# Optimization experiments

Hardware: AMD Instinct MI355X
Metric: run time of the kernel (lower is better)

## Reference

```python
import jax, jax.numpy as jnp
import numpy as np

N = 50000
E = 600000
IN_DIM = 2000
HID = 64
OUT_DIM = 25
HEADS = 4
NHEAD = 4
NLAYERS = 2
FF = 2048
EPS = 1e-5


def gat_conv(x, W, a_src, a_dst, b, src, dst, heads, out_dim):
    n = x.shape[0]
    h = (x @ W).reshape(n, heads, out_dim)
    # per-node attention logits
    al_src = jnp.sum(h * a_src[None], axis=-1)  # [N,H]
    al_dst = jnp.sum(h * a_dst[None], axis=-1)  # [N,H]
    e = jax.nn.leaky_relu(al_src[src] + al_dst[dst], negative_slope=0.2)  # [E,H]
    # segment softmax over destination nodes (every node has a self-loop)
    m = jax.ops.segment_max(e, dst, num_segments=n)
    ex = jnp.exp(e - m[dst])
    s = jax.ops.segment_sum(ex, dst, num_segments=n)
    alpha = ex / (s[dst] + 1e-16)  # [E,H]
    msg = h[src] * alpha[..., None]  # [E,H,out]
    out = jax.ops.segment_sum(msg, dst, num_segments=n)  # [N,H,out]
    return out.reshape(n, heads * out_dim) + b


def layer_norm(x, g, b):
    mu = jnp.mean(x, axis=-1, keepdims=True)
    var = jnp.mean(jnp.square(x - mu), axis=-1, keepdims=True)
    return (x - mu) * jax.lax.rsqrt(var + EPS) * g + b


def encoder_layer(x, Wq, Wk, Wv, bq, bk, bv, Wo, bo, g1, b1, Wf1, bf1, Wf2, bf2, g2, b2):
    # seq_len = 1: each node is its own length-1 sequence -> softmax weights are 1
    n, d = x.shape
    dh = d // NHEAD
    q = (x @ Wq + bq).reshape(n, NHEAD, dh)
    k = (x @ Wk + bk).reshape(n, NHEAD, dh)
    v = (x @ Wv + bv).reshape(n, NHEAD, dh)
    s = jnp.sum(q * k, axis=-1, keepdims=True) / jnp.sqrt(jnp.float32(dh))  # [N,H,1]
    a = jax.nn.softmax(s, axis=-1)  # all ones (length-1 softmax)
    attn = (a * v).reshape(n, d) @ Wo + bo
    x = layer_norm(x + attn, g1, b1)
    ff = jax.nn.relu(x @ Wf1 + bf1) @ Wf2 + bf2
    return layer_norm(x + ff, g2, b2)


def setup_inputs() -> dict:
    key = jax.random.key(0)
    ks = jax.random.split(key, 40)
    sc = 0.05
    inp = {}
    inp["x"] = jax.random.normal(ks[0], (N, IN_DIM), dtype=jnp.float32)
    inp["edge_src"] = jax.random.randint(ks[1], (E,), 0, N, dtype=jnp.int32)
    inp["edge_dst"] = jax.random.randint(ks[2], (E,), 0, N, dtype=jnp.int32)
    # GAT layer 1: in -> hidden, heads=4
    inp["W1"] = jax.random.normal(ks[3], (IN_DIM, HEADS * HID), dtype=jnp.float32) * sc
    inp["a_src1"] = jax.random.normal(ks[4], (HEADS, HID), dtype=jnp.float32) * sc
    inp["a_dst1"] = jax.random.normal(ks[5], (HEADS, HID), dtype=jnp.float32) * sc
    inp["b1"] = jnp.zeros((HEADS * HID,), dtype=jnp.float32)
    # GAT layer 2: hidden*heads -> hidden, heads=1
    inp["W2"] = jax.random.normal(ks[6], (HEADS * HID, HID), dtype=jnp.float32) * sc
    inp["a_src2"] = jax.random.normal(ks[7], (1, HID), dtype=jnp.float32) * sc
    inp["a_dst2"] = jax.random.normal(ks[8], (1, HID), dtype=jnp.float32) * sc
    inp["b2"] = jnp.zeros((HID,), dtype=jnp.float32)
    # Transformer fusion params, stacked over layers
    def pl(k, shape):
        return jax.random.normal(k, shape, dtype=jnp.float32) * sc
    inp["t_Wq"] = pl(ks[9], (NLAYERS, HID, HID))
    inp["t_Wk"] = pl(ks[10], (NLAYERS, HID, HID))
    inp["t_Wv"] = pl(ks[11], (NLAYERS, HID, HID))
    inp["t_bq"] = jnp.zeros((NLAYERS, HID), dtype=jnp.float32)
    inp["t_bk"] = jnp.zeros((NLAYERS, HID), dtype=jnp.float32)
    inp["t_bv"] = jnp.zeros((NLAYERS, HID), dtype=jnp.float32)
    inp["t_Wo"] = pl(ks[12], (NLAYERS, HID, HID))
    inp["t_bo"] = jnp.zeros((NLAYERS, HID), dtype=jnp.float32)
    inp["t_ln1g"] = jnp.ones((NLAYERS, HID), dtype=jnp.float32)
    inp["t_ln1b"] = jnp.zeros((NLAYERS, HID), dtype=jnp.float32)
    inp["t_Wff1"] = pl(ks[13], (NLAYERS, HID, FF))
    inp["t_bff1"] = jnp.zeros((NLAYERS, FF), dtype=jnp.float32)
    inp["t_Wff2"] = pl(ks[14], (NLAYERS, FF, HID))
    inp["t_bff2"] = jnp.zeros((NLAYERS, HID), dtype=jnp.float32)
    inp["t_ln2g"] = jnp.ones((NLAYERS, HID), dtype=jnp.float32)
    inp["t_ln2b"] = jnp.zeros((NLAYERS, HID), dtype=jnp.float32)
    # GAT ADT head: hidden -> out, heads=1
    inp["W3"] = pl(ks[15], (HID, OUT_DIM))
    inp["a_src3"] = pl(ks[16], (1, OUT_DIM))
    inp["a_dst3"] = pl(ks[17], (1, OUT_DIM))
    inp["b3"] = jnp.zeros((OUT_DIM,), dtype=jnp.float32)
    return inp


def reference(x, edge_src, edge_dst, W1, a_src1, a_dst1, b1, W2, a_src2, a_dst2, b2,
              t_Wq, t_Wk, t_Wv, t_bq, t_bk, t_bv, t_Wo, t_bo, t_ln1g, t_ln1b,
              t_Wff1, t_bff1, t_Wff2, t_bff2, t_ln2g, t_ln2b,
              W3, a_src3, a_dst3, b3):
    # add self-loops (PyG GATConv default add_self_loops=True)
    loops = jnp.arange(N, dtype=edge_src.dtype)
    src = jnp.concatenate([edge_src, loops])
    dst = jnp.concatenate([edge_dst, loops])

    h = gat_conv(x, W1, a_src1, a_dst1, b1, src, dst, HEADS, HID)
    h = jax.nn.elu(h)
    rna = gat_conv(h, W2, a_src2, a_dst2, b2, src, dst, 1, HID)
    rna = jax.nn.elu(rna)

    fused = rna
    for l in range(NLAYERS):
        fused = encoder_layer(fused, t_Wq[l], t_Wk[l], t_Wv[l], t_bq[l], t_bk[l], t_bv[l],
                              t_Wo[l], t_bo[l], t_ln1g[l], t_ln1b[l],
                              t_Wff1[l], t_bff1[l], t_Wff2[l], t_bff2[l],
                              t_ln2g[l], t_ln2b[l])

    adt_pred = gat_conv(fused, W3, a_src3, a_dst3, b3, src, dst, 1, OUT_DIM)
    return (adt_pred, fused)
```

## Files before the change

### kernel.cpp

```cpp
#include <hip/hip_runtime.h>
#include <math.h>

#define N_NODES 50000
#define IN_DIMC 2000
#define FF_DIM 2048
#define EPSV 1e-5f
#define SCAN_B 1024

typedef __attribute__((ext_vector_type(8))) short sh8;
typedef __attribute__((ext_vector_type(4))) short sh4;
typedef __attribute__((ext_vector_type(4))) float f32x4;

__device__ __forceinline__ void splitf(float f, unsigned short& h, unsigned short& l) {
    unsigned u = __float_as_uint(f);
    h = (unsigned short)(u >> 16);
    float fh = __uint_as_float(u & 0xFFFF0000u);
    l = (unsigned short)(__float_as_uint(f - fh) >> 16);
}

__global__ void k_zero_i32(int* p, int n) {
    int i = blockIdx.x * blockDim.x + threadIdx.x;
    if (i < n) p[i] = 0;
}

__global__ void k_hist(const int* __restrict__ dst, int* __restrict__ deg, int E, int n) {
    int i = blockIdx.x * blockDim.x + threadIdx.x;
    if (i < E + n) {
        int d = (i < E) ? dst[i] : (i - E);
        atomicAdd(&deg[d], 1);
    }
}

__global__ __launch_bounds__(1024) void k_scan1(const int* __restrict__ deg, int* __restrict__ rstart,
                                                int* __restrict__ part, int n) {
    __shared__ int lds[SCAN_B];
    int t = threadIdx.x;
    int base = blockIdx.x * SCAN_B;
    int v = (base + t < n) ? deg[base + t] : 0;
    lds[t] = v;
    __syncthreads();
    for (int o = 1; o < SCAN_B; o <<= 1) {
        int add = (t >= o) ? lds[t - o] : 0;
        __syncthreads();
        lds[t] += add;
        __syncthreads();
    }
    if (base + t < n) rstart[base + t] = lds[t] - v;
    if (t == SCAN_B - 1) part[blockIdx.x] = lds[t];
}

__global__ void k_scan2(int* part, int nb) {
    if (threadIdx.x == 0 && blockIdx.x == 0) {
        int s = 0;
        for (int i = 0; i < nb; i++) { int v = part[i]; part[i] = s; s += v; }
    }
}

__global__ void k_scan3(int* rstart, const int* __restrict__ part, int n) {
    int i = blockIdx.x * blockDim.x + threadIdx.x;
    if (i < n) rstart[i] += part[i / SCAN_B];
}

__global__ void k_scatter(const int* __restrict__ src, const int* __restrict__ dst,
                          const int* __restrict__ rstart, int* __restrict__ cursor,
                          int* __restrict__ csr_src, int E, int n) {
    int i = blockIdx.x * blockDim.x + threadIdx.x;
    if (i < E + n) {
        int s, d;
        if (i < E) { s = src[i]; d = dst[i]; } else { s = i - E; d = s; }
        int pos = rstart[d] + atomicAdd(&cursor[d], 1);
        csr_src[pos] = s;
    }
}

__global__ void k_wsplit(const float* __restrict__ W, short* __restrict__ oh,
                         short* __restrict__ ol, int K, int N) {
    int i = blockIdx.x * blockDim.x + threadIdx.x;
    if (i < K * N) {
        int k = i / N, c = i - k * N;
        unsigned short h, l;
        splitf(W[i], h, l);
        oh[(size_t)c * K + k] = (short)h;
        ol[(size_t)c * K + k] = (short)l;
    }
}

__global__ __launch_bounds__(256, 2) void k_gemm_sb(const float* __restrict__ A,
                                                    const short* __restrict__ Bth,
                                                    const short* __restrict__ Btl,
                                                    float* __restrict__ C, int M, int N, int K) {
    __shared__ short lds[36864];
    short* Ah = lds;
    short* Al = lds + 9216;
    short* Bh = lds + 18432;
    short* Bl = lds + 27648;
    int tid = threadIdx.x;
    int wave = tid >> 6, lane = tid & 63;
    int wm = wave & 1, wn = wave >> 1;
    int l15 = lane & 15, l4 = lane >> 4;
    long m0 = (long)blockIdx.x * 128;
    int n0 = blockIdx.y * 128;
    f32x4 acc[4][4] = {};
    int ktiles = (K + 63) >> 6;
    for (int kt = 0; kt < ktiles; kt++) {
        int k0 = kt << 6;
#pragma unroll
        for (int p = 0; p < 8; p++) {
            int f4 = tid + p * 256;
            int row = f4 >> 4, kq = f4 & 15;
            long gm = m0 + row;
            int gk = k0 + kq * 4;
            float4 a = {0.f, 0.f, 0.f, 0.f};
            if (gm < M && gk < K) a = *(const float4*)&A[gm * K + gk];
            unsigned short h0, h1, h2, h3, l0, l1, l2, l3;
            splitf(a.x, h0, l0); splitf(a.y, h1, l1);
            splitf(a.z, h2, l2); splitf(a.w, h3, l3);
            sh4 hv = {(short)h0, (short)h1, (short)h2, (short)h3};
            sh4 lv = {(short)l0, (short)l1, (short)l2, (short)l3};
            *(sh4*)&Ah[row * 72 + kq * 4] = hv;
            *(sh4*)&Al[row * 72 + kq * 4] = lv;
        }
#pragma unroll
        for (int p = 0; p < 4; p++) {
            int u = tid + p * 256;
            int col = u >> 3, kq8 = u & 7;
            int gk = k0 + kq8 * 8;
            int gc = n0 + col;
            sh8 bh8 = {0, 0, 0, 0, 0, 0, 0, 0}, bl8 = {0, 0, 0, 0, 0, 0, 0, 0};
            if (gk < K) {
                bh8 = *(const sh8*)&Bth[(size_t)gc * K + gk];
                bl8 = *(const sh8*)&Btl[(size_t)gc * K + gk];
            }
            *(sh8*)&Bh[col * 72 + kq8 * 8] = bh8;
            *(sh8*)&Bl[col * 72 + kq8 * 8] = bl8;
        }
        __syncthreads();
#pragma unroll
        for (int kf = 0; kf < 2; kf++) {
            sh8 ah[4], alv[4], bh[4], blv[4];
#pragma unroll
            for (int mf = 0; mf < 4; mf++) {
                int off = (wm * 64 + mf * 16 + l15) * 72 + kf * 32 + l4 * 8;
                ah[mf] = *(const sh8*)&Ah[off];
                alv[mf] = *(const sh8*)&Al[off];
            }
#pragma unroll
            for (int nf = 0; nf < 4; nf++) {
                int off = (wn * 64 + nf * 16 + l15) * 72 + kf * 32 + l4 * 8;
                bh[nf] = *(const sh8*)&Bh[off];
                blv[nf] = *(const sh8*)&Bl[off];
            }
#pragma unroll
            for (int mf = 0; mf < 4; mf++)
#pragma unroll
                for (int nf = 0; nf < 4; nf++) {
                    f32x4 c = acc[mf][nf];
                    c = __builtin_amdgcn_mfma_f32_16x16x32_bf16(ah[mf], bh[nf], c, 0, 0, 0);
                    c = __builtin_amdgcn_mfma_f32_16x16x32_bf16(ah[mf], blv[nf], c, 0, 0, 0);
                    c = __builtin_amdgcn_mfma_f32_16x16x32_bf16(alv[mf], bh[nf], c, 0, 0, 0);
                    acc[mf][nf] = c;
                }
        }
        __syncthreads();
    }
#pragma unroll
    for (int mf = 0; mf < 4; mf++)
#pragma unroll
        for (int r = 0; r < 4; r++) {
            long gm = m0 + wm * 64 + mf * 16 + l4 * 4 + r;
            if (gm >= M) continue;
#pragma unroll
            for (int nf = 0; nf < 4; nf++) {
                int gc = n0 + wn * 64 + nf * 16 + l15;
                C[gm * N + gc] = acc[mf][nf][r];
            }
        }
}

__global__ __launch_bounds__(256, 2) void k_ff_mfma(const float* __restrict__ x,
                                                    const short* __restrict__ W1h, const short* __restrict__ W1l,
                                                    const float* __restrict__ bf1,
                                                    const short* __restrict__ W2h, const short* __restrict__ W2l,
                                                    const float* __restrict__ bf2,
                                                    float* __restrict__ out, int n) {
    __shared__ short lds[36864];
    short* Hh = lds;
    short* Hl = lds + 9216;
    short* w1h = lds + 18432;
    short* w1l = lds + 23040;
    short* w2h = lds + 27648;
    short* w2l = lds + 32256;
    int tid = threadIdx.x;
    int wave = tid >> 6, lane = tid & 63;
    int wm = wave & 1, wn = wave >> 1;
    int l15 = lane & 15, l4 = lane >> 4;
    long row0 = (long)blockIdx.x * 128;
#pragma unroll
    for (int p = 0; p < 8; p++) {
        int f4 = tid + p * 256;
        int row = f4 >> 4, kq = f4 & 15;
        long gr = row0 + row;
        float4 a = {0.f, 0.f, 0.f, 0.f};
        if (gr < n) a = *(const float4*)&x[gr * 64 + kq * 4];
        unsigned short h0, h1, h2, h3, l0, l1, l2, l3;
        splitf(a.x, h0, l0); splitf(a.y, h1, l1);
        splitf(a.z, h2, l2); splitf(a.w, h3, l3);
        sh4 hv = {(short)h0, (short)h1, (short)h2, (short)h3};
        sh4 lv = {(short)l0, (short)l1, (short)l2, (short)l3};
        *(sh4*)&Hh[row * 72 + kq * 4] = hv;
        *(sh4*)&Hl[row * 72 + kq * 4] = lv;
    }
    __syncthreads();
    sh8 xh[4][2], xl[4][2];
#pragma unroll
    for (int mf = 0; mf < 4; mf++)
#pragma unroll
        for (int kf = 0; kf < 2; kf++) {
            int off = (wm * 64 + mf * 16 + l15) * 72 + kf * 32 + l4 * 8;
            xh[mf][kf] = *(const sh8*)&Hh[off];
            xl[mf][kf] = *(const sh8*)&Hl[off];
        }
    f32x4 acc2[4][2] = {};
    for (int j0 = 0; j0 < FF_DIM; j0 += 64) {
#pragma unroll
        for (int p = 0; p < 2; p++) {
            int u = tid + p * 256;
            int cj = u >> 3, kq8 = u & 7;
            *(sh8*)&w1h[cj * 72 + kq8 * 8] = *(const sh8*)&W1h[(size_t)(j0 + cj) * 64 + kq8 * 8];
            *(sh8*)&w1l[cj * 72 + kq8 * 8] = *(const sh8*)&W1l[(size_t)(j0 + cj) * 64 + kq8 * 8];
            *(sh8*)&w2h[cj * 72 + kq8 * 8] = *(const sh8*)&W2h[(size_t)cj * FF_DIM + j0 + kq8 * 8];
            *(sh8*)&w2l[cj * 72 + kq8 * 8] = *(const sh8*)&W2l[(size_t)cj * FF_DIM + j0 + kq8 * 8];
        }
        __syncthreads();
        f32x4 hacc[4][2] = {};
#pragma unroll
        for (int kf = 0; kf < 2; kf++) {
            sh8 bh[2], bl[2];
#pragma unroll
            for (int nf = 0; nf < 2; nf++) {
                int off = (wn * 32 + nf * 16 + l15) * 72 + kf * 32 + l4 * 8;
                bh[nf] = *(const sh8*)&w1h[off];
                bl[nf] = *(const sh8*)&w1l[off];
            }
#pragma unroll
            for (int mf = 0; mf < 4; mf++)
#pragma unroll
                for (int nf = 0; nf < 2; nf++) {
                    f32x4 c = hacc[mf][nf];
                    c = __builtin_amdgcn_mfma_f32_16x16x32_bf16(xh[mf][kf], bh[nf], c, 0, 0, 0);
                    c = __builtin_amdgcn_mfma_f32_16x16x32_bf16(xh[mf][kf], bl[nf], c, 0, 0, 0);
                    c = __builtin_amdgcn_mfma_f32_16x16x32_bf16(xl[mf][kf], bh[nf], c, 0, 0, 0);
                    hacc[mf][nf] = c;
                }
        }
#pragma unroll
        for (int mf = 0; mf < 4; mf++)
#pragma unroll
            for (int nf = 0; nf < 2; nf++) {
                int col = wn * 32 + nf * 16 + l15;
                float b1v = bf1[j0 + col];
#pragma unroll
                for (int r = 0; r < 4; r++) {
                    int row = wm * 64 + mf * 16 + l4 * 4 + r;
                    float v = fmaxf(hacc[mf][nf][r] + b1v, 0.f);
                    unsigned short h, l;
                    splitf(v, h, l);
                    Hh[row * 72 + col] = (short)h;
                    Hl[row * 72 + col] = (short)l;
                }
            }
        __syncthreads();
#pragma unroll
        for (int kf = 0; kf < 2; kf++) {
            sh8 ah[4], alv[4], bh[2], bl[2];
#pragma unroll
            for (int mf = 0; mf < 4; mf++) {
                int off = (wm * 64 + mf * 16 + l15) * 72 + kf * 32 + l4 * 8;
                ah[mf] = *(const sh8*)&Hh[off];
                alv[mf] = *(const sh8*)&Hl[off];
            }
#pragma unroll
            for (int nf = 0; nf < 2; nf++) {
                int off = (wn * 32 + nf * 16 + l15) * 72 + kf * 32 + l4 * 8;
                bh[nf] = *(const sh8*)&w2h[off];
                bl[nf] = *(const sh8*)&w2l[off];
            }
#pragma unroll
            for (int mf = 0; mf < 4; mf++)
#pragma unroll
                for (int nf = 0; nf < 2; nf++) {
                    f32x4 c = acc2[mf][nf];
                    c = __builtin_amdgcn_mfma_f32_16x16x32_bf16(ah[mf], bh[nf], c, 0, 0, 0);
                    c = __builtin_amdgcn_mfma_f32_16x16x32_bf16(ah[mf], bl[nf], c, 0, 0, 0);
                    c = __builtin_amdgcn_mfma_f32_16x16x32_bf16(alv[mf], bh[nf], c, 0, 0, 0);
                    acc2[mf][nf] = c;
                }
        }
        __syncthreads();
    }
#pragma unroll
    for (int mf = 0; mf < 4; mf++)
#pragma unroll
        for (int r = 0; r < 4; r++) {
            long gr = row0 + wm * 64 + mf * 16 + l4 * 4 + r;
            if (gr >= n) continue;
#pragma unroll
            for (int nf = 0; nf < 2; nf++) {
                int gc = wn * 32 + nf * 16 + l15;
                out[gr * 64 + gc] = acc2[mf][nf][r] + bf2[gc];
            }
        }
}

template<int BM, int BN, int BK, int CS>
__global__ __launch_bounds__(256) void k_gemm(const float* __restrict__ A, const float* __restrict__ B,
                                              const float* __restrict__ bias, float* __restrict__ C,
                                              int M, int N, int K) {
    __shared__ float As[BK][BM + 4];
    __shared__ float Bs[BK][BN + 4];
    int tid = threadIdx.x;
    long m0 = (long)blockIdx.x * BM;
    int n0 = blockIdx.y * BN;
    int tc = tid & 15, tr = tid >> 4;
    float acc[2][CS][4][4] = {};
    for (int k0 = 0; k0 < K; k0 += BK) {
        constexpr int APASS = BM * BK / 1024;
#pragma unroll
        for (int p = 0; p < APASS; p++) {
            int f4 = tid + p * 256;
            int kq = f4 % (BK / 4);
            int row = f4 / (BK / 4);
            long gm = m0 + row;
            float4 a = {0.f, 0.f, 0.f, 0.f};
            if (gm < M) a = *(const float4*)&A[gm * K + k0 + kq * 4];
            As[kq * 4 + 0][row] = a.x;
            As[kq * 4 + 1][row] = a.y;
            As[kq * 4 + 2][row] = a.z;
            As[kq * 4 + 3][row] = a.w;
        }
        constexpr int BPASS = BK * BN / 1024;
#pragma unroll
        for (int p = 0; p < BPASS; p++) {
            int f4 = tid + p * 256;
            int c4 = f4 % (BN / 4);
            int kr = f4 / (BN / 4);
            int gc = n0 + c4 * 4;
            const float* brow = &B[(size_t)(k0 + kr) * N];
            float4 b;
            if ((N & 3) == 0 && gc + 3 < N) {
                b = *(const float4*)&brow[gc];
            } else {
                float t0[4] = {0.f, 0.f, 0.f, 0.f};
                for (int i = 0; i < 4; i++)
                    if (gc + i < N) t0[i] = brow[gc + i];
                b.x = t0[0]; b.y = t0[1]; b.z = t0[2]; b.w = t0[3];
            }
            *(float4*)&Bs[kr][c4 * 4] = b;
        }
        __syncthreads();
#pragma unroll
        for (int k = 0; k < BK; k++) {
            float av[2][4], bv[CS][4];
            float4 a0 = *(const float4*)&As[k][4 * tr];
            float4 a1 = *(const float4*)&As[k][BM / 2 + 4 * tr];
            av[0][0] = a0.x; av[0][1] = a0.y; av[0][2] = a0.z; av[0][3] = a0.w;
            av[1][0] = a1.x; av[1][1] = a1.y; av[1][2] = a1.z; av[1][3] = a1.w;
            float4 b0 = *(const float4*)&Bs[k][4 * tc];
            bv[0][0] = b0.x; bv[0][1] = b0.y; bv[0][2] = b0.z; bv[0][3] = b0.w;
            if (CS == 2) {
                float4 b1 = *(const float4*)&Bs[k][BN / 2 + 4 * tc];
                bv[1][0] = b1.x; bv[1][1] = b1.y; bv[1][2] = b1.z; bv[1][3] = b1.w;
            }
#pragma unroll
            for (int rs = 0; rs < 2; rs++)
#pragma unroll
                for (int cs = 0; cs < CS; cs++)
#pragma unroll
                    for (int i = 0; i < 4; i++)
#pragma unroll
                        for (int j = 0; j < 4; j++)
                            acc[rs][cs][i][j] += av[rs][i] * bv[cs][j];
        }
        __syncthreads();
    }
#pragma unroll
    for (int rs = 0; rs < 2; rs++)
        for (int i = 0; i < 4; i++) {
            long gm = m0 + rs * (BM / 2) + 4 * tr + i;
            if (gm >= M) continue;
            for (int cs = 0; cs < CS; cs++)
                for (int j = 0; j < 4; j++) {
                    int gc = n0 + cs * (BN / 2) + 4 * tc + j;
                    if (gc >= N) continue;
                    float v = acc[rs][cs][i][j];
                    if (bias) v += bias[gc];
                    C[gm * N + gc] = v;
                }
        }
}

template<int H, int D>
__global__ void k_al(const float* __restrict__ h, const float* __restrict__ a_src,
                     const float* __restrict__ a_dst, float* __restrict__ als,
                     float* __restrict__ ald, int n) {
    long w = ((long)blockIdx.x * blockDim.x + threadIdx.x) >> 6;
    int lane = threadIdx.x & 63;
    long nn = w / H;
    int hh = (int)(w % H);
    if (nn >= n) return;
    float v = 0.f, u = 0.f;
    if (lane < D) {
        float hv = h[nn * (H * D) + hh * D + lane];
        v = hv * a_src[hh * D + lane];
        u = hv * a_dst[hh * D + lane];
    }
#pragma unroll
    for (int o = 32; o > 0; o >>= 1) {
        v += __shfl_xor(v, o, 64);
        u += __shfl_xor(u, o, 64);
    }
    if (lane == 0) { als[nn * H + hh] = v; ald[nn * H + hh] = u; }
}

template<int H, int D, bool DO_ELU>
__global__ __launch_bounds__(256) void k_gat_agg(const float* __restrict__ h, const float* __restrict__ als,
                                                 const float* __restrict__ ald, const float* __restrict__ bias,
                                                 const int* __restrict__ rstart, const int* __restrict__ deg,
                                                 const int* __restrict__ csr_src, float* __restrict__ out) {
    const int CH = 64;
    __shared__ float wbuf[CH][H];
    __shared__ int sbuf[CH];
    int n = blockIdx.x;
    int tid = threadIdx.x;
    int hh = (D == 64) ? (tid >> 6) : (tid / D);
    int d = (D == 64) ? (tid & 63) : (tid % D);
    bool act = tid < H * D;
    int beg = rstart[n];
    int cnt = deg[n];
    float acc = 0.f, wsum = 0.f;
    for (int c0 = 0; c0 < cnt; c0 += CH) {
        int rem = min(CH, cnt - c0);
        if (tid < CH * H) {
            int ei = tid & (CH - 1);
            int h2 = tid >> 6;
            if (ei < rem) {
                int s = csr_src[beg + c0 + ei];
                if (h2 == 0) sbuf[ei] = s;
                float l = als[s * H + h2] + ald[n * H + h2];
                l = (l > 0.f) ? l : 0.2f * l;
                wbuf[ei][h2] = __expf(l);
            }
        }
        __syncthreads();
        if (act) {
            for (int ei = 0; ei < rem; ei++) {
                int s = sbuf[ei];
                float w = wbuf[ei][hh];
                wsum += w;
                acc += w * h[(size_t)s * (H * D) + hh * D + d];
            }
        }
        __syncthreads();
    }
    if (act) {
        float v = acc / (wsum + 1e-16f) + bias[hh * D + d];
        if (DO_ELU) v = (v > 0.f) ? v : expm1f(v);
        out[(size_t)n * (H * D) + hh * D + d] = v;
    }
}

__global__ void k_ln(const float* __restrict__ x, const float* __restrict__ y,
                     const float* __restrict__ g, const float* __restrict__ b,
                     float* __restrict__ out, int n) {
    long w = ((long)blockIdx.x * blockDim.x + threadIdx.x) >> 6;
    int lane = threadIdx.x & 63;
    if (w >= n) return;
    float v = x[w * 64 + lane] + y[w * 64 + lane];
    float s = v;
#pragma unroll
    for (int o = 32; o > 0; o >>= 1) s += __shfl_xor(s, o, 64);
    float mu = s * (1.f / 64.f);
    float dv = v - mu;
    float q = dv * dv;
#pragma unroll
    for (int o = 32; o > 0; o >>= 1) q += __shfl_xor(q, o, 64);
    float var = q * (1.f / 64.f);
    out[w * 64 + lane] = dv * rsqrtf(var + EPSV) * g[lane] + b[lane];
}

extern "C" void kernel_launch(void* const* d_in, const int* in_sizes, int n_in,
                              void* d_out, int out_size, void* d_ws, size_t ws_size,
                              hipStream_t stream) {
    const float* x = (const float*)d_in[0];
    const int* esrc = (const int*)d_in[1];
    const int* edst = (const int*)d_in[2];
    const float* W1 = (const float*)d_in[3];
    const float* as1 = (const float*)d_in[4];
    const float* ad1 = (const float*)d_in[5];
    const float* b1 = (const float*)d_in[6];
    const float* W2 = (const float*)d_in[7];
    const float* as2 = (const float*)d_in[8];
    const float* ad2 = (const float*)d_in[9];
    const float* b2 = (const float*)d_in[10];
    const float* tWv = (const float*)d_in[13];
    const float* tbv = (const float*)d_in[16];
    const float* tWo = (const float*)d_in[17];
    const float* tbo = (const float*)d_in[18];
    const float* tg1 = (const float*)d_in[19];
    const float* tb1 = (const float*)d_in[20];
    const float* tWf1 = (const float*)d_in[21];
    const float* tbf1 = (const float*)d_in[22];
    const float* tWf2 = (const float*)d_in[23];
    const float* tbf2 = (const float*)d_in[24];
    const float* tg2 = (const float*)d_in[25];
    const float* tb2 = (const float*)d_in[26];
    const float* W3 = (const float*)d_in[27];
    const float* as3 = (const float*)d_in[28];
    const float* ad3 = (const float*)d_in[29];
    const float* b3 = (const float*)d_in[30];

    const int n = N_NODES;
    const int E = in_sizes[1];
    const int ET = E + n;

    float* fw = (float*)d_ws;
    float* h1 = fw;
    float* agg1 = h1 + 12800000;
    float* bufA = agg1 + 12800000;
    float* bufB = bufA + 3200000;
    float* bufC = bufB + 3200000;
    float* bufD = bufC + 3200000;
    float* als = bufD + 3200000;
    float* ald = als + 200000;
    float* h3 = h1;
    int* deg = (int*)(ald + 200000);
    int* rstart = deg + 50016;
    int* cursor = rstart + 50016;
    int* part = cursor + 50016;
    int* csr = part + 64;

    short* w1th = (short*)agg1;
    short* w1tl = w1th + 512000;
    short* wfb = (short*)(h1 + 8000000);
    const size_t WFS = 131072;
    short* wf1h = wfb;
    short* wf1l = wfb + 2 * WFS;
    short* wf2h = wfb + 4 * WFS;
    short* wf2l = wfb + 6 * WFS;

    float* outAdt = (float*)d_out;
    float* outFused = outAdt + (size_t)n * 25;

    k_zero_i32<<<(150048 + 255) / 256, 256, 0, stream>>>(deg, 150048);
    k_hist<<<(ET + 255) / 256, 256, 0, stream>>>(edst, deg, E, n);
    int nsb = (n + SCAN_B - 1) / SCAN_B;
    k_scan1<<<nsb, SCAN_B, 0, stream>>>(deg, rstart, part, n);
    k_scan2<<<1, 64, 0, stream>>>(part, nsb);
    k_scan3<<<(n + 255) / 256, 256, 0, stream>>>(rstart, part, n);
    k_scatter<<<(ET + 255) / 256, 256, 0, stream>>>(esrc, edst, rstart, cursor, csr, E, n);

    k_wsplit<<<(512000 + 255) / 256, 256, 0, stream>>>(W1, w1th, w1tl, IN_DIMC, 256);
    k_gemm_sb<<<dim3((n + 127) / 128, 2), 256, 0, stream>>>(x, w1th, w1tl, h1, n, 256, IN_DIMC);
    k_al<4, 64><<<n, 256, 0, stream>>>(h1, as1, ad1, als, ald, n);
    k_gat_agg<4, 64, true><<<n, 256, 0, stream>>>(h1, als, ald, b1, rstart, deg, csr, agg1);

    for (int l = 0; l < 2; l++) {
        k_wsplit<<<(131072 + 255) / 256, 256, 0, stream>>>(tWf1 + (size_t)l * 64 * FF_DIM,
                                                           wf1h + l * WFS, wf1l + l * WFS, 64, FF_DIM);
        k_wsplit<<<(131072 + 255) / 256, 256, 0, stream>>>(tWf2 + (size_t)l * FF_DIM * 64,
                                                           wf2h + l * WFS, wf2l + l * WFS, FF_DIM, 64);
    }

    k_gemm<128, 64, 16, 1><<<dim3((n + 127) / 128, 1), 256, 0, stream>>>(agg1, W2, nullptr, bufA, n, 64, 256);
    k_al<1, 64><<<(n + 3) / 4, 256, 0, stream>>>(bufA, as2, ad2, als, ald, n);
    k_gat_agg<1, 64, true><<<n, 64, 0, stream>>>(bufA, als, ald, b2, rstart, deg, csr, bufB);

    float* xin = bufB;
    for (int l = 0; l < 2; l++) {
        const float* Wv = tWv + (size_t)l * 64 * 64;
        const float* bv = tbv + (size_t)l * 64;
        const float* Wo = tWo + (size_t)l * 64 * 64;
        const float* bo = tbo + (size_t)l * 64;
        k_gemm<128, 64, 16, 1><<<dim3((n + 127) / 128, 1), 256, 0, stream>>>(xin, Wv, bv, bufC, n, 64, 64);
        k_gemm<128, 64, 16, 1><<<dim3((n + 127) / 128, 1), 256, 0, stream>>>(bufC, Wo, bo, bufD, n, 64, 64);
        k_ln<<<(n + 3) / 4, 256, 0, stream>>>(xin, bufD, tg1 + (size_t)l * 64, tb1 + (size_t)l * 64, bufA, n);
        k_ff_mfma<<<(n + 127) / 128, 256, 0, stream>>>(bufA, wf1h + l * WFS, wf1l + l * WFS,
                                                       tbf1 + (size_t)l * FF_DIM,
                                                       wf2h + l * WFS, wf2l + l * WFS,
                                                       tbf2 + (size_t)l * 64, bufC, n);
        float* xout = (l == 1) ? outFused : bufB;
        k_ln<<<(n + 3) / 4, 256, 0, stream>>>(bufA, bufC, tg2 + (size_t)l * 64, tb2 + (size_t)l * 64, xout, n);
        xin = xout;
    }

    k_gemm<128, 64, 16, 1><<<dim3((n + 127) / 128, 1), 256, 0, stream>>>(outFused, W3, nullptr, h3, n, 25, 64);
    k_al<1, 25><<<(n + 3) / 4, 256, 0, stream>>>(h3, as3, ad3, als, ald, n);
    k_gat_agg<1, 25, false><<<n, 64, 0, stream>>>(h3, als, ald, b3, rstart, deg, csr, outAdt);
}
```

Measured before the change: 1.626 ms.

## Use direct-to-LDS split-bf16 MFMA GEMM everywhere, fold Wv·Wo, warp-per-node GAT aggregation

```diff
diff --git a/kernel.cpp b/kernel.cpp
--- a/kernel.cpp
+++ b/kernel.cpp
@@ -16,6 +16,25 @@
     h = (unsigned short)(u >> 16);
     float fh = __uint_as_float(u & 0xFFFF0000u);
     l = (unsigned short)(__float_as_uint(f - fh) >> 16);
+}
+
+__device__ __forceinline__ void split8(f32x4 a0, f32x4 a1, sh8& hh, sh8& ll) {
+    float f[8] = {a0[0], a0[1], a0[2], a0[3], a1[0], a1[1], a1[2], a1[3]};
+    sh8 h, l;
+#pragma unroll
+    for (int j = 0; j < 8; j++) {
+        unsigned u = __float_as_uint(f[j]);
+        h[j] = (short)(u >> 16);
+        float fhi = __uint_as_float(u & 0xFFFF0000u);
+        l[j] = (short)(__float_as_uint(f[j] - fhi) >> 16);
+    }
+    hh = h; ll = l;
+}
+
+__device__ __forceinline__ void gload_lds16(const float* g, float* l) {
+    __builtin_amdgcn_global_load_lds(
+        (const __attribute__((address_space(1))) unsigned int*)g,
+        (__attribute__((address_space(3))) unsigned int*)l, 16, 0, 0);
 }
 
 __global__ void k_zero_i32(int* p, int n) {
@@ -73,6 +92,18 @@
     }
 }
 
+__global__ void k_wsplit_pad(const float* __restrict__ W, short* __restrict__ oh,
+                             short* __restrict__ ol, int K, int N, int Kpad, int Npad) {
+    int i = blockIdx.x * blockDim.x + threadIdx.x;
+    if (i < Kpad * Npad) {
+        int c = i / Kpad, k = i - c * Kpad;
+        float v = (c < N && k < K) ? W[(size_t)k * N + c] : 0.f;
+        unsigned short h, l;
+        splitf(v, h, l);
+        oh[i] = (short)h; ol[i] = (short)l;
+    }
+}
+
 __global__ void k_wsplit(const float* __restrict__ W, short* __restrict__ oh,
                          short* __restrict__ ol, int K, int N) {
     int i = blockIdx.x * blockDim.x + threadIdx.x;
@@ -85,81 +116,98 @@
     }
 }
 
-__global__ __launch_bounds__(256, 2) void k_gemm_sb(const float* __restrict__ A,
-                                                    const short* __restrict__ Bth,
-                                                    const short* __restrict__ Btl,
-                                                    float* __restrict__ C, int M, int N, int K) {
-    __shared__ short lds[36864];
-    short* Ah = lds;
-    short* Al = lds + 9216;
-    short* Bh = lds + 18432;
-    short* Bl = lds + 27648;
+__global__ void k_wcomb(const float* __restrict__ Wv, const float* __restrict__ bv,
+                        const float* __restrict__ Wo, const float* __restrict__ bo,
+                        short* __restrict__ och, short* __restrict__ ocl, float* __restrict__ bc) {
+    int i = blockIdx.x * blockDim.x + threadIdx.x;
+    if (i < 4096) {
+        int cc = i & 63, kk = i >> 6;
+        float s = 0.f;
+        for (int j = 0; j < 64; j++) s += Wv[kk * 64 + j] * Wo[j * 64 + cc];
+        unsigned short h, l;
+        splitf(s, h, l);
+        och[cc * 64 + kk] = (short)h;
+        ocl[cc * 64 + kk] = (short)l;
+        if (kk == 0) {
+            float t = bo[cc];
+            for (int j = 0; j < 64; j++) t += bv[j] * Wo[j * 64 + cc];
+            bc[cc] = t;
+        }
+    }
+}
+
+template<int NF>
+__global__ __launch_bounds__(256, 2) void k_gemm_x(const float* __restrict__ A,
+                                                   const short* __restrict__ Bth,
+                                                   const short* __restrict__ Btl,
+                                                   const float* __restrict__ bias,
+                                                   float* __restrict__ C,
+                                                   int M, int N, int K, int Kpad) {
+    constexpr int BN = NF * 32;
+    __shared__ float Afs[128 * 64];
+    __shared__ short Bhs[BN * 64];
+    __shared__ short Bls[BN * 64];
     int tid = threadIdx.x;
     int wave = tid >> 6, lane = tid & 63;
     int wm = wave & 1, wn = wave >> 1;
     int l15 = lane & 15, l4 = lane >> 4;
     long m0 = (long)blockIdx.x * 128;
-    int n0 = blockIdx.y * 128;
-    f32x4 acc[4][4] = {};
-    int ktiles = (K + 63) >> 6;
+    int n0 = blockIdx.y * BN;
+    int chunks = K >> 2;
+    int cmax = chunks - 1;
+    int ktiles = (chunks + 15) >> 4;
+    f32x4 acc[4][NF] = {};
+    int Sl = wave * 512 + lane;
     for (int kt = 0; kt < ktiles; kt++) {
-        int k0 = kt << 6;
-#pragma unroll
-        for (int p = 0; p < 8; p++) {
-            int f4 = tid + p * 256;
-            int row = f4 >> 4, kq = f4 & 15;
-            long gm = m0 + row;
-            int gk = k0 + kq * 4;
-            float4 a = {0.f, 0.f, 0.f, 0.f};
-            if (gm < M && gk < K) a = *(const float4*)&A[gm * K + gk];
-            unsigned short h0, h1, h2, h3, l0, l1, l2, l3;
-            splitf(a.x, h0, l0); splitf(a.y, h1, l1);
-            splitf(a.z, h2, l2); splitf(a.w, h3, l3);
-            sh4 hv = {(short)h0, (short)h1, (short)h2, (short)h3};
-            sh4 lv = {(short)l0, (short)l1, (short)l2, (short)l3};
-            *(sh4*)&Ah[row * 72 + kq * 4] = hv;
-            *(sh4*)&Al[row * 72 + kq * 4] = lv;
-        }
-#pragma unroll
-        for (int p = 0; p < 4; p++) {
+        int c0 = kt << 4;
+#pragma unroll
+        for (int i = 0; i < 8; i++) {
+            int S = Sl + i * 64;
+            int row = S >> 4, slot = S & 15;
+            long srcrow = m0 + row; if (srcrow > (long)M - 1) srcrow = M - 1;
+            int ch = c0 + (slot ^ (row & 7)); if (ch > cmax) ch = cmax;
+            gload_lds16(A + (size_t)srcrow * K + (size_t)ch * 4,
+                        &Afs[(wave * 512 + i * 64) * 4]);
+        }
+#pragma unroll
+        for (int p = 0; p < NF; p++) {
             int u = tid + p * 256;
-            int col = u >> 3, kq8 = u & 7;
-            int gk = k0 + kq8 * 8;
-            int gc = n0 + col;
-            sh8 bh8 = {0, 0, 0, 0, 0, 0, 0, 0}, bl8 = {0, 0, 0, 0, 0, 0, 0, 0};
-            if (gk < K) {
-                bh8 = *(const sh8*)&Bth[(size_t)gc * K + gk];
-                bl8 = *(const sh8*)&Btl[(size_t)gc * K + gk];
-            }
-            *(sh8*)&Bh[col * 72 + kq8 * 8] = bh8;
-            *(sh8*)&Bl[col * 72 + kq8 * 8] = bl8;
+            int col = u >> 3, k8 = u & 7;
+            size_t src = (size_t)(n0 + col) * Kpad + (size_t)kt * 64 + k8 * 8;
+            sh8 bh = *(const sh8*)&Bth[src];
+            sh8 bl = *(const sh8*)&Btl[src];
+            int doff = col * 64 + ((k8 ^ (col & 7)) << 3);
+            *(sh8*)&Bhs[doff] = bh;
+            *(sh8*)&Bls[doff] = bl;
         }
         __syncthreads();
 #pragma unroll
         for (int kf = 0; kf < 2; kf++) {
-            sh8 ah[4], alv[4], bh[4], blv[4];
+            sh8 ah[4], al[4];
 #pragma unroll
             for (int mf = 0; mf < 4; mf++) {
-                int off = (wm * 64 + mf * 16 + l15) * 72 + kf * 32 + l4 * 8;
-                ah[mf] = *(const sh8*)&Ah[off];
-                alv[mf] = *(const sh8*)&Al[off];
-            }
-#pragma unroll
-            for (int nf = 0; nf < 4; nf++) {
-                int off = (wn * 64 + nf * 16 + l15) * 72 + kf * 32 + l4 * 8;
-                bh[nf] = *(const sh8*)&Bh[off];
-                blv[nf] = *(const sh8*)&Bl[off];
-            }
-#pragma unroll
-            for (int mf = 0; mf < 4; mf++)
-#pragma unroll
-                for (int nf = 0; nf < 4; nf++) {
+                int row = wm * 64 + mf * 16 + l15;
+                int s0 = kf * 8 + l4 * 2;
+                f32x4 a0 = *(const f32x4*)&Afs[row * 64 + ((s0 ^ (row & 7)) << 2)];
+                f32x4 a1 = *(const f32x4*)&Afs[row * 64 + (((s0 + 1) ^ (row & 7)) << 2)];
+                split8(a0, a1, ah[mf], al[mf]);
+            }
+#pragma unroll
+            for (int nf = 0; nf < NF; nf++) {
+                int col = wn * (NF * 16) + nf * 16 + l15;
+                int k8 = kf * 4 + l4;
+                int boff = col * 64 + ((k8 ^ (col & 7)) << 3);
+                sh8 bh = *(const sh8*)&Bhs[boff];
+                sh8 bl = *(const sh8*)&Bls[boff];
+#pragma unroll
+                for (int mf = 0; mf < 4; mf++) {
                     f32x4 c = acc[mf][nf];
-                    c = __builtin_amdgcn_mfma_f32_16x16x32_bf16(ah[mf], bh[nf], c, 0, 0, 0);
-                    c = __builtin_amdgcn_mfma_f32_16x16x32_bf16(ah[mf], blv[nf], c, 0, 0, 0);
-                    c = __builtin_amdgcn_mfma_f32_16x16x32_bf16(alv[mf], bh[nf], c, 0, 0, 0);
+                    c = __builtin_amdgcn_mfma_f32_16x16x32_bf16(ah[mf], bh, c, 0, 0, 0);
+                    c = __builtin_amdgcn_mfma_f32_16x16x32_bf16(ah[mf], bl, c, 0, 0, 0);
+                    c = __builtin_amdgcn_mfma_f32_16x16x32_bf16(al[mf], bh, c, 0, 0, 0);
                     acc[mf][nf] = c;
                 }
+            }
         }
         __syncthreads();
     }
@@ -170,9 +218,9 @@
             long gm = m0 + wm * 64 + mf * 16 + l4 * 4 + r;
             if (gm >= M) continue;
 #pragma unroll
-            for (int nf = 0; nf < 4; nf++) {
-                int gc = n0 + wn * 64 + nf * 16 + l15;
-                C[gm * N + gc] = acc[mf][nf][r];
+            for (int nf = 0; nf < NF; nf++) {
+                int gc = n0 + wn * (NF * 16) + nf * 16 + l15;
+                if (gc < N) C[gm * (size_t)N + gc] = acc[mf][nf][r] + (bias ? bias[gc] : 0.f);
             }
         }
 }
@@ -312,93 +360,6 @@
         }
 }
 
-template<int BM, int BN, int BK, int CS>
-__global__ __launch_bounds__(256) void k_gemm(const float* __restrict__ A, const float* __restrict__ B,
-                                              const float* __restrict__ bias, float* __restrict__ C,
-                                              int M, int N, int K) {
-    __shared__ float As[BK][BM + 4];
-    __shared__ float Bs[BK][BN + 4];
-    int tid = threadIdx.x;
-    long m0 = (long)blockIdx.x * BM;
-    int n0 = blockIdx.y * BN;
-    int tc = tid & 15, tr = tid >> 4;
-    float acc[2][CS][4][4] = {};
-    for (int k0 = 0; k0 < K; k0 += BK) {
-        constexpr int APASS = BM * BK / 1024;
-#pragma unroll
-        for (int p = 0; p < APASS; p++) {
-            int f4 = tid + p * 256;
-            int kq = f4 % (BK / 4);
-            int row = f4 / (BK / 4);
-            long gm = m0 + row;
-            float4 a = {0.f, 0.f, 0.f, 0.f};
-            if (gm < M) a = *(const float4*)&A[gm * K + k0 + kq * 4];
-            As[kq * 4 + 0][row] = a.x;
-            As[kq * 4 + 1][row] = a.y;
-            As[kq * 4 + 2][row] = a.z;
-            As[kq * 4 + 3][row] = a.w;
-        }
-        constexpr int BPASS = BK * BN / 1024;
-#pragma unroll
-        for (int p = 0; p < BPASS; p++) {
-            int f4 = tid + p * 256;
-            int c4 = f4 % (BN / 4);
-            int kr = f4 / (BN / 4);
-            int gc = n0 + c4 * 4;
-            const float* brow = &B[(size_t)(k0 + kr) * N];
-            float4 b;
-            if ((N & 3) == 0 && gc + 3 < N) {
-                b = *(const float4*)&brow[gc];
-            } else {
-                float t0[4] = {0.f, 0.f, 0.f, 0.f};
-                for (int i = 0; i < 4; i++)
-                    if (gc + i < N) t0[i] = brow[gc + i];
-                b.x = t0[0]; b.y = t0[1]; b.z = t0[2]; b.w = t0[3];
-            }
-            *(float4*)&Bs[kr][c4 * 4] = b;
-        }
-        __syncthreads();
-#pragma unroll
-        for (int k = 0; k < BK; k++) {
-            float av[2][4], bv[CS][4];
-            float4 a0 = *(const float4*)&As[k][4 * tr];
-            float4 a1 = *(const float4*)&As[k][BM / 2 + 4 * tr];
-            av[0][0] = a0.x; av[0][1] = a0.y; av[0][2] = a0.z; av[0][3] = a0.w;
-            av[1][0] = a1.x; av[1][1] = a1.y; av[1][2] = a1.z; av[1][3] = a1.w;
-            float4 b0 = *(const float4*)&Bs[k][4 * tc];
-            bv[0][0] = b0.x; bv[0][1] = b0.y; bv[0][2] = b0.z; bv[0][3] = b0.w;
-            if (CS == 2) {
-                float4 b1 = *(const float4*)&Bs[k][BN / 2 + 4 * tc];
-                bv[1][0] = b1.x; bv[1][1] = b1.y; bv[1][2] = b1.z; bv[1][3] = b1.w;
-            }
-#pragma unroll
-            for (int rs = 0; rs < 2; rs++)
-#pragma unroll
-                for (int cs = 0; cs < CS; cs++)
-#pragma unroll
-                    for (int i = 0; i < 4; i++)
-#pragma unroll
-                        for (int j = 0; j < 4; j++)
-                            acc[rs][cs][i][j] += av[rs][i] * bv[cs][j];
-        }
-        __syncthreads();
-    }
-#pragma unroll
-    for (int rs = 0; rs < 2; rs++)
-        for (int i = 0; i < 4; i++) {
-            long gm = m0 + rs * (BM / 2) + 4 * tr + i;
-            if (gm >= M) continue;
-            for (int cs = 0; cs < CS; cs++)
-                for (int j = 0; j < 4; j++) {
-                    int gc = n0 + cs * (BN / 2) + 4 * tc + j;
-                    if (gc >= N) continue;
-                    float v = acc[rs][cs][i][j];
-                    if (bias) v += bias[gc];
-                    C[gm * N + gc] = v;
-                }
-        }
-}
-
 template<int H, int D>
 __global__ void k_al(const float* __restrict__ h, const float* __restrict__ a_src,
                      const float* __restrict__ a_dst, float* __restrict__ als,
@@ -423,49 +384,48 @@
 }
 
 template<int H, int D, bool DO_ELU>
-__global__ __launch_bounds__(256) void k_gat_agg(const float* __restrict__ h, const float* __restrict__ als,
-                                                 const float* __restrict__ ald, const float* __restrict__ bias,
-                                                 const int* __restrict__ rstart, const int* __restrict__ deg,
-                                                 const int* __restrict__ csr_src, float* __restrict__ out) {
-    const int CH = 64;
-    __shared__ float wbuf[CH][H];
-    __shared__ int sbuf[CH];
-    int n = blockIdx.x;
-    int tid = threadIdx.x;
-    int hh = (D == 64) ? (tid >> 6) : (tid / D);
-    int d = (D == 64) ? (tid & 63) : (tid % D);
-    bool act = tid < H * D;
-    int beg = rstart[n];
-    int cnt = deg[n];
-    float acc = 0.f, wsum = 0.f;
-    for (int c0 = 0; c0 < cnt; c0 += CH) {
-        int rem = min(CH, cnt - c0);
-        if (tid < CH * H) {
-            int ei = tid & (CH - 1);
-            int h2 = tid >> 6;
-            if (ei < rem) {
-                int s = csr_src[beg + c0 + ei];
-                if (h2 == 0) sbuf[ei] = s;
-                float l = als[s * H + h2] + ald[n * H + h2];
-                l = (l > 0.f) ? l : 0.2f * l;
-                wbuf[ei][h2] = __expf(l);
-            }
-        }
-        __syncthreads();
-        if (act) {
-            for (int ei = 0; ei < rem; ei++) {
-                int s = sbuf[ei];
-                float w = wbuf[ei][hh];
-                wsum += w;
-                acc += w * h[(size_t)s * (H * D) + hh * D + d];
-            }
-        }
-        __syncthreads();
-    }
-    if (act) {
-        float v = acc / (wsum + 1e-16f) + bias[hh * D + d];
-        if (DO_ELU) v = (v > 0.f) ? v : expm1f(v);
-        out[(size_t)n * (H * D) + hh * D + d] = v;
+__global__ __launch_bounds__(256) void k_gat_agg_w(const float* __restrict__ h,
+                                                   const float* __restrict__ als,
+                                                   const float* __restrict__ ald,
+                                                   const float* __restrict__ bias,
+                                                   const int* __restrict__ rstart,
+                                                   const int* __restrict__ deg,
+                                                   const int* __restrict__ csr_src,
+                                                   float* __restrict__ out, int n) {
+    int wid = (int)(((long)blockIdx.x * blockDim.x + threadIdx.x) >> 6);
+    int lane = threadIdx.x & 63;
+    if (wid >= n) return;
+    int beg = rstart[wid], cnt = deg[wid];
+    float aldv = 0.f;
+    if (lane < H) aldv = ald[wid * H + lane];
+    float wsum = 0.f;
+    float acc[H];
+#pragma unroll
+    for (int i = 0; i < H; i++) acc[i] = 0.f;
+    for (int e = 0; e < cnt; e++) {
+        int s = csr_src[beg + e];
+        float w = 0.f;
+        if (lane < H) {
+            float lg = als[s * H + lane] + aldv;
+            lg = (lg > 0.f) ? lg : 0.2f * lg;
+            w = __expf(lg);
+            wsum += w;
+        }
+#pragma unroll
+        for (int hh = 0; hh < H; hh++) {
+            float wv = __shfl(w, hh, 64);
+            float hv = (lane < D) ? h[(size_t)s * (H * D) + hh * D + lane] : 0.f;
+            acc[hh] += wv * hv;
+        }
+    }
+#pragma unroll
+    for (int hh = 0; hh < H; hh++) {
+        float ws = __shfl(wsum, hh, 64);
+        if (lane < D) {
+            float v = acc[hh] / (ws + 1e-16f) + bias[hh * D + lane];
+            if (DO_ELU) v = (v > 0.f) ? v : expm1f(v);
+            out[(size_t)wid * (H * D) + hh * D + lane] = v;
+        }
     }
 }
 
@@ -525,28 +485,34 @@
 
     float* fw = (float*)d_ws;
     float* h1 = fw;
-    float* agg1 = h1 + 12800000;
-    float* bufA = agg1 + 12800000;
-    float* bufB = bufA + 3200000;
-    float* bufC = bufB + 3200000;
-    float* bufD = bufC + 3200000;
-    float* als = bufD + 3200000;
-    float* ald = als + 200000;
-    float* h3 = h1;
-    int* deg = (int*)(ald + 200000);
+    float* agg1 = fw + 12800000;
+    float* bufA = fw + 25600000;
+    float* bufB = fw + 28800000;
+    float* bufC = fw + 32000000;
+    float* bufD = fw + 35200000;
+    float* als = fw + 38400000;
+    float* ald = fw + 38600000;
+    float* bc = fw + 38800000;
+    int* deg = (int*)(fw + 38800064);
     int* rstart = deg + 50016;
     int* cursor = rstart + 50016;
     int* part = cursor + 50016;
     int* csr = part + 64;
-
-    short* w1th = (short*)agg1;
-    short* w1tl = w1th + 512000;
-    short* wfb = (short*)(h1 + 8000000);
+    short* sbase = (short*)(csr + 700000);
+    short* w1th = sbase;
+    short* w1tl = w1th + 524288;
+    short* w2th = w1tl + 524288;
+    short* w2tl = w2th + 16384;
+    short* w3th = w2tl + 16384;
+    short* w3tl = w3th + 4096;
+    short* wcth = w3tl + 4096;
+    short* wctl = wcth + 4096;
     const size_t WFS = 131072;
-    short* wf1h = wfb;
-    short* wf1l = wfb + 2 * WFS;
-    short* wf2h = wfb + 4 * WFS;
-    short* wf2l = wfb + 6 * WFS;
+    short* wf1h = wctl + 4096;
+    short* wf1l = wf1h + 2 * WFS;
+    short* wf2h = wf1l + 2 * WFS;
+    short* wf2l = wf2h + 2 * WFS;
+    float* h3 = h1;
 
     float* outAdt = (float*)d_out;
     float* outFused = outAdt + (size_t)n * 25;
@@ -559,11 +525,9 @@
     k_scan3<<<(n + 255) / 256, 256, 0, stream>>>(rstart, part, n);
     k_scatter<<<(ET + 255) / 256, 256, 0, stream>>>(esrc, edst, rstart, cursor, csr, E, n);
 
-    k_wsplit<<<(512000 + 255) / 256, 256, 0, stream>>>(W1, w1th, w1tl, IN_DIMC, 256);
-    k_gemm_sb<<<dim3((n + 127) / 128, 2), 256, 0, stream>>>(x, w1th, w1tl, h1, n, 256, IN_DIMC);
-    k_al<4, 64><<<n, 256, 0, stream>>>(h1, as1, ad1, als, ald, n);
-    k_gat_agg<4, 64, true><<<n, 256, 0, stream>>>(h1, als, ald, b1, rstart, deg, csr, agg1);
-
+    k_wsplit_pad<<<(524288 + 255) / 256, 256, 0, stream>>>(W1, w1th, w1tl, IN_DIMC, 256, 2048, 256);
+    k_wsplit_pad<<<(16384 + 255) / 256, 256, 0, stream>>>(W2, w2th, w2tl, 256, 64, 256, 64);
+    k_wsplit_pad<<<(4096 + 255) / 256, 256, 0, stream>>>(W3, w3th, w3tl, 64, 25, 64, 64);
     for (int l = 0; l < 2; l++) {
         k_wsplit<<<(131072 + 255) / 256, 256, 0, stream>>>(tWf1 + (size_t)l * 64 * FF_DIM,
                                                            wf1h + l * WFS, wf1l + l * WFS, 64, FF_DIM);
@@ -571,18 +535,20 @@
                                                            wf2h + l * WFS, wf2l + l * WFS, FF_DIM, 64);
     }
 
-    k_gemm<128, 64, 16, 1><<<dim3((n + 127) / 128, 1), 256, 0, stream>>>(agg1, W2, nullptr, bufA, n, 64, 256);
+    k_gemm_x<4><<<dim3((n + 127) / 128, 2), 256, 0, stream>>>(x, w1th, w1tl, nullptr, h1, n, 256, IN_DIMC, 2048);
+    k_al<4, 64><<<n, 256, 0, stream>>>(h1, as1, ad1, als, ald, n);
+    k_gat_agg_w<4, 64, true><<<(n + 3) / 4, 256, 0, stream>>>(h1, als, ald, b1, rstart, deg, csr, agg1, n);
+
+    k_gemm_x<2><<<dim3((n + 127) / 128, 1), 256, 0, stream>>>(agg1, w2th, w2tl, nullptr, bufA, n, 64, 256, 256);
     k_al<1, 64><<<(n + 3) / 4, 256, 0, stream>>>(bufA, as2, ad2, als, ald, n);
-    k_gat_agg<1, 64, true><<<n, 64, 0, stream>>>(bufA, als, ald, b2, rstart, deg, csr, bufB);
+    k_gat_agg_w<1, 64, true><<<(n + 3) / 4, 256, 0, stream>>>(bufA, als, ald, b2, rstart, deg, csr, bufB, n);
 
     float* xin = bufB;
     for (int l = 0; l < 2; l++) {
-        const float* Wv = tWv + (size_t)l * 64 * 64;
-        const float* bv = tbv + (size_t)l * 64;
-        const float* Wo = tWo + (size_t)l * 64 * 64;
-        const float* bo = tbo + (size_t)l * 64;
-        k_gemm<128, 64, 16, 1><<<dim3((n + 127) / 128, 1), 256, 0, stream>>>(xin, Wv, bv, bufC, n, 64, 64);
-        k_gemm<128, 64, 16, 1><<<dim3((n + 127) / 128, 1), 256, 0, stream>>>(bufC, Wo, bo, bufD, n, 64, 64);
+        k_wcomb<<<16, 256, 0, stream>>>(tWv + (size_t)l * 4096, tbv + (size_t)l * 64,
+                                        tWo + (size_t)l * 4096, tbo + (size_t)l * 64,
+                                        wcth, wctl, bc);
+        k_gemm_x<2><<<dim3((n + 127) / 128, 1), 256, 0, stream>>>(xin, wcth, wctl, bc, bufD, n, 64, 64, 64);
         k_ln<<<(n + 3) / 4, 256, 0, stream>>>(xin, bufD, tg1 + (size_t)l * 64, tb1 + (size_t)l * 64, bufA, n);
         k_ff_mfma<<<(n + 127) / 128, 256, 0, stream>>>(bufA, wf1h + l * WFS, wf1l + l * WFS,
                                                        tbf1 + (size_t)l * FF_DIM,
@@ -593,7 +559,7 @@
         xin = xout;
     }
 
-    k_gemm<128, 64, 16, 1><<<dim3((n + 127) / 128, 1), 256, 0, stream>>>(outFused, W3, nullptr, h3, n, 25, 64);
+    k_gemm_x<2><<<dim3((n + 127) / 128, 1), 256, 0, stream>>>(outFused, w3th, w3tl, nullptr, h3, n, 25, 64, 64);
     k_al<1, 25><<<(n + 3) / 4, 256, 0, stream>>>(h3, as3, ad3, als, ald, n);
-    k_gat_agg<1, 25, false><<<n, 64, 0, stream>>>(h3, als, ald, b3, rstart, deg, csr, outAdt);
-}
+    k_gat_agg_w<1, 25, false><<<(n + 3) / 4, 256, 0, stream>>>(h3, als, ald, b3, rstart, deg, csr, outAdt, n);
+}
```

Result: faster. 1.484 ms (-8.7%).
